# Kernel optimization log

Measured on AMD Instinct MI355X. Metric: run time of the kernel, lower is better.

The kernel has to match this reference:

```python
import jax, jax.numpy as jnp
import numpy as np

B = 16384          # batch_size / n_samples
SRC = 200          # source_num
C = 10             # category_size
I = SRC * C        # input_size = 2000
EPS = 1e-10


def setup_inputs() -> dict:
    key = jax.random.key(0)
    ks = jax.random.split(key, 8)
    # forward data
    x = jax.random.uniform(ks[0], (B, I), dtype=jnp.float32)
    mask = jax.random.uniform(ks[1], (B, I), dtype=jnp.float32)
    y_target = jax.random.uniform(ks[2], (B, C), dtype=jnp.float32)
    # learned parameters (xavier-uniform style init)
    def xavier(k, shape):
        fan_in, fan_out = shape[0], shape[1]
        limit = float(np.sqrt(2.0)) * float(np.sqrt(6.0 / (fan_in + fan_out)))
        return jax.random.uniform(k, shape, dtype=jnp.float32, minval=-limit, maxval=limit)
    W_reconstr = xavier(ks[3], (C, I))
    b_reconstr = xavier(ks[4], (1, I))
    W_yc = xavier(ks[5], (I, C))
    b_yc = xavier(ks[6], (1, C))
    return {"x": x, "mask": mask, "y_target": y_target,
            "W_reconstr": W_reconstr, "b_reconstr": b_reconstr,
            "W_yc": W_yc, "b_yc": b_yc}


def reference(x, mask, y_target, W_reconstr, b_reconstr, W_yc, b_yc):
    # ---- decoder (collapsed): constant_y[i] is a batch of identical one-hot
    # rows at category i, so y @ W_reconstr + b == W_reconstr[i] + b for all
    # batch elements. Stack over all i -> logits [C, I].
    logits = W_reconstr + b_reconstr                      # [C, I]
    e = jnp.exp(logits).reshape(C, SRC, C)                # per-source blocks
    # block-diagonal matmul == segmented sum over each source's C entries
    p = (e / e.sum(axis=-1, keepdims=True)).reshape(C, I)  # [C, I]
    logp = jnp.log(EPS + p)                               # [C, I]
    # -mean_j(mask * x * log p_i) per category i -> [B, C]
    reconstr_x = -(x * mask) @ logp.T / I

    # ---- encoder
    y_classifier = jax.nn.softmax(x @ W_yc + b_yc, axis=1)  # [B, C]

    # ---- losses
    loss_w_l1 = jnp.sum(jnp.abs(W_yc))
    loss_classifier_y_x = jnp.mean(jnp.sum(y_classifier * reconstr_x, axis=1))
    loss_y_kl = jnp.mean(jnp.sum(
        y_classifier * (jnp.log(EPS + y_classifier) - jnp.log(EPS + y_target)),
        axis=1))
    loss = (loss_classifier_y_x + 1e-4 * loss_y_kl
            + 0.005 / SRC / C / C * loss_w_l1)
    return (y_classifier, loss)
```

## Files before the change

kernel.cpp:

```cpp
#include <hip/hip_runtime.h>
#include <hip/hip_bf16.h>

#define B_SZ 16384
#define SRCN 200
#define CAT  10
#define IN   2000
#define QCOL 500
#define QPAD 512
#define TQB  10240
#define EPSF 1e-10f

typedef _Float16 half2v __attribute__((ext_vector_type(2)));

#if __has_builtin(__builtin_amdgcn_fdot2)
__device__ __forceinline__ float fdot2(half2v a, half2v b, float c) {
    return __builtin_amdgcn_fdot2(a, b, c, false);
}
#else
__device__ __forceinline__ float fdot2(half2v a, half2v b, float c) {
    return c + (float)a[0] * (float)b[0] + (float)a[1] * (float)b[1];
}
#endif

__device__ __forceinline__ half2v pkrtz(float a, float b) {
#if __has_builtin(__builtin_amdgcn_cvt_pkrtz)
    union { __fp16 __attribute__((ext_vector_type(2))) i; half2v o; } v;
    v.i = __builtin_amdgcn_cvt_pkrtz(a, b);
    return v.o;
#else
    half2v r; r[0] = (_Float16)a; r[1] = (_Float16)b; return r;
#endif
}

__device__ __forceinline__ half2v as_h2(unsigned u) {
    union { unsigned u; half2v h; } v; v.u = u; return v.h;
}

__device__ __forceinline__ short f2h(float f) {
    union { _Float16 h; short s; } v; v.h = (_Float16)f; return v.s;
}

__global__ void prep_kernel(const float* __restrict__ W_rec,
                            const float* __restrict__ b_rec,
                            const float* __restrict__ W_yc,
                            short* __restrict__ lp4,
                            short* __restrict__ wy4,
                            double* __restrict__ acc) {
    if (blockIdx.x == gridDim.x - 1) {
        float p = 0.f;
        for (int i = threadIdx.x; i < IN * CAT; i += blockDim.x) p += fabsf(W_yc[i]);
        __shared__ float red[4];
        for (int o = 32; o; o >>= 1) p += __shfl_down(p, o, 64);
        if ((threadIdx.x & 63) == 0) red[threadIdx.x >> 6] = p;
        __syncthreads();
        if (threadIdx.x == 0) {
            acc[0] = 0.0; acc[1] = 0.0;
            acc[2] = (double)(red[0] + red[1] + red[2] + red[3]);
        }
        return;
    }
    int idx = blockIdx.x * blockDim.x + threadIdx.x;
    int q   = idx / (CAT * QPAD);
    int rem = idx % (CAT * QPAD);
    int n   = rem >> 9;
    int kk  = rem & 511;
    short wv = 0, lv = 0;
    if (kk < QCOL) {
        int k = q * QCOL + kk;
        wv = f2h(W_yc[k * CAT + n]);
        int base = (k / CAT) * CAT;
        float lg[CAT];
        float m = -1e30f;
        #pragma unroll
        for (int i = 0; i < CAT; i++) {
            lg[i] = W_rec[n * IN + base + i] + b_rec[base + i];
            m = fmaxf(m, lg[i]);
        }
        float s = 0.f;
        #pragma unroll
        for (int i = 0; i < CAT; i++) s += expf(lg[i] - m);
        float myl = W_rec[n * IN + k] + b_rec[k];
        float pp = expf(myl - m) / s;
        lv = f2h(logf(EPSF + pp));
    }
    lp4[idx] = lv;
    wy4[idx] = wv;
}

__global__ __launch_bounds__(256, 4) void main_kernel(
        const float* __restrict__ x, const float* __restrict__ mask,
        const short* __restrict__ lp4, const short* __restrict__ wy4,
        float* __restrict__ part) {
    __shared__ __attribute__((aligned(16))) char lds[2 * TQB];

    const int q = blockIdx.x & 3;
    {
        const uint4* s1 = (const uint4*)(lp4 + q * (CAT * QPAD));
        const uint4* s2 = (const uint4*)(wy4 + q * (CAT * QPAD));
        uint4* d1 = (uint4*)lds;
        uint4* d2 = (uint4*)(lds + TQB);
        #pragma unroll
        for (int i = 0; i < 3; ++i) {
            int j = i * 256 + threadIdx.x;
            if (j < 640) { d1[j] = s1[j]; d2[j] = s2[j]; }
        }
    }
    __syncthreads();

    const int l  = threadIdx.x & 63;
    const int w  = threadIdx.x >> 6;
    const int g  = l >> 4;
    const int li = l & 15;
    const int row = (blockIdx.x >> 2) * 16 + w * 4 + g;

    const int col0 = q * QCOL + li * 4;
    const float* xr = x + (size_t)row * IN + col0;
    const float* mr = mask + (size_t)row * IN + col0;

    float4 xv[8], mv[8];
    #pragma unroll
    for (int cc = 0; cc < 7; ++cc) {
        xv[cc] = *(const float4*)(xr + cc * 64);
        mv[cc] = *(const float4*)(mr + cc * 64);
    }
    {
        const int base = col0 + 7 * 64;
        const int adj = (base > IN - 4) ? (base - (IN - 4)) : 0;
        xv[7] = *(const float4*)(xr + 7 * 64 - adj);
        mv[7] = *(const float4*)(mr + 7 * 64 - adj);
    }

    float pR[CAT], pW[CAT];
    #pragma unroll
    for (int c = 0; c < CAT; ++c) { pR[c] = 0.f; pW[c] = 0.f; }

    #pragma unroll
    for (int cc = 0; cc < 8; ++cc) {
        const half2v ax0 = pkrtz(xv[cc].x, xv[cc].y);
        const half2v ax1 = pkrtz(xv[cc].z, xv[cc].w);
        const half2v am0 = pkrtz(xv[cc].x * mv[cc].x, xv[cc].y * mv[cc].y);
        const half2v am1 = pkrtz(xv[cc].z * mv[cc].z, xv[cc].w * mv[cc].w);
        const int tb = cc * 128 + li * 8;
        #pragma unroll
        for (int c = 0; c < CAT; ++c) {
            const uint2 lpv = *(const uint2*)(lds + c * 1024 + tb);
            const uint2 wyv = *(const uint2*)(lds + TQB + c * 1024 + tb);
            pR[c] = fdot2(am0, as_h2(lpv.x), pR[c]);
            pR[c] = fdot2(am1, as_h2(lpv.y), pR[c]);
            pW[c] = fdot2(ax0, as_h2(wyv.x), pW[c]);
            pW[c] = fdot2(ax1, as_h2(wyv.y), pW[c]);
        }
    }

    #pragma unroll
    for (int c = 0; c < CAT; ++c) {
        #pragma unroll
        for (int o = 1; o < 16; o <<= 1) {
            pR[c] += __shfl_xor(pR[c], o, 64);
            pW[c] += __shfl_xor(pW[c], o, 64);
        }
    }
    if (li == 0) {
        float* pp = part + ((size_t)row * 4 + q) * 20;
        #pragma unroll
        for (int c = 0; c < CAT; ++c) { pp[c] = pR[c]; pp[10 + c] = pW[c]; }
    }
}

__global__ void combine_kernel(const float* __restrict__ part,
                               const float* __restrict__ y_target,
                               const float* __restrict__ b_yc,
                               float* __restrict__ out,
                               double* __restrict__ acc) {
    const int row = blockIdx.x * 256 + threadIdx.x;
    const float* pp = part + (size_t)row * 80;
    float pR[CAT], pW[CAT];
    #pragma unroll
    for (int c = 0; c < CAT; ++c) {
        pR[c] = pp[c] + pp[20 + c] + pp[40 + c] + pp[60 + c];
        pW[c] = pp[10 + c] + pp[30 + c] + pp[50 + c] + pp[70 + c] + b_yc[c];
    }
    float mx = -1e30f;
    #pragma unroll
    for (int c = 0; c < CAT; ++c) mx = fmaxf(mx, pW[c]);
    float y[CAT], s = 0.f;
    #pragma unroll
    for (int c = 0; c < CAT; ++c) { y[c] = __expf(pW[c] - mx); s += y[c]; }
    const float is = 1.f / s;
    float cls = 0.f, kl = 0.f;
    float* op = out + (size_t)row * CAT;
    #pragma unroll
    for (int c = 0; c < CAT; ++c) {
        y[c] *= is;
        op[c] = y[c];
        cls += y[c] * (-pR[c] * (1.f / IN));
        const float yt = y_target[(size_t)row * CAT + c];
        kl += y[c] * (__logf(EPSF + y[c]) - __logf(EPSF + yt));
    }
    #pragma unroll
    for (int o = 32; o; o >>= 1) {
        cls += __shfl_down(cls, o, 64);
        kl  += __shfl_down(kl, o, 64);
    }
    __shared__ float rc[4], rk[4];
    if ((threadIdx.x & 63) == 0) {
        rc[threadIdx.x >> 6] = cls; rk[threadIdx.x >> 6] = kl;
    }
    __syncthreads();
    if (threadIdx.x == 0) {
        atomicAdd(&acc[0], (double)(rc[0] + rc[1] + rc[2] + rc[3]));
        atomicAdd(&acc[1], (double)(rk[0] + rk[1] + rk[2] + rk[3]));
    }
}

__global__ void final_kernel(const double* __restrict__ acc,
                             float* __restrict__ out) {
    if (threadIdx.x == 0) {
        double loss = acc[0] / (double)B_SZ
                    + 1e-4 * (acc[1] / (double)B_SZ)
                    + (0.005 / (double)SRCN / (double)CAT / (double)CAT) * acc[2];
        out[(size_t)B_SZ * CAT] = (float)loss;
    }
}

extern "C" void kernel_launch(void* const* d_in, const int* in_sizes, int n_in,
                              void* d_out, int out_size, void* d_ws, size_t ws_size,
                              hipStream_t stream) {
    const float* x        = (const float*)d_in[0];
    const float* mask     = (const float*)d_in[1];
    const float* y_target = (const float*)d_in[2];
    const float* W_rec    = (const float*)d_in[3];
    const float* b_rec    = (const float*)d_in[4];
    const float* W_yc     = (const float*)d_in[5];
    const float* b_yc     = (const float*)d_in[6];
    float* out  = (float*)d_out;
    double* acc = (double*)d_ws;
    short* lp4  = (short*)((char*)d_ws + 256);
    short* wy4  = lp4 + 4 * CAT * QPAD;
    float* part = (float*)((char*)d_ws + 256 + 2 * 40960);

    prep_kernel<<<81, 256, 0, stream>>>(W_rec, b_rec, W_yc, lp4, wy4, acc);
    main_kernel<<<4096, 256, 0, stream>>>(x, mask, lp4, wy4, part);
    combine_kernel<<<64, 256, 0, stream>>>(part, y_target, b_yc, out, acc);
    final_kernel<<<1, 64, 0, stream>>>(acc, out);
}
```

Measured before the change: 72.99 us.

## Persistent-style main kernel with double-buffered row-tile prefetch

The main kernel drops from 4096 to 1024 blocks, and each block now handles four row tiles in a loop. The x and mask loads are split into two halves that are double-buffered, so the next tile's global loads are issued while the current half computes. Scheduling barriers pin the order. This spreads the LDS table staging over more work and hides memory latency, at the cost of higher register pressure and fewer blocks in flight.

```diff
diff --git a/kernel.cpp b/kernel.cpp
--- a/kernel.cpp
+++ b/kernel.cpp
@@ -8,6 +8,7 @@
 #define QCOL 500
 #define QPAD 512
 #define TQB  10240
+#define NBLK 1024
 #define EPSF 1e-10f
 
 typedef _Float16 half2v __attribute__((ext_vector_type(2)));
@@ -111,59 +112,88 @@
     const int w  = threadIdx.x >> 6;
     const int g  = l >> 4;
     const int li = l & 15;
-    const int row = (blockIdx.x >> 2) * 16 + w * 4 + g;
-
+    const int rt0 = blockIdx.x >> 2;
     const int col0 = q * QCOL + li * 4;
-    const float* xr = x + (size_t)row * IN + col0;
-    const float* mr = mask + (size_t)row * IN + col0;
-
-    float4 xv[8], mv[8];
-    #pragma unroll
-    for (int cc = 0; cc < 7; ++cc) {
-        xv[cc] = *(const float4*)(xr + cc * 64);
-        mv[cc] = *(const float4*)(mr + cc * 64);
-    }
-    {
-        const int base = col0 + 7 * 64;
-        const int adj = (base > IN - 4) ? (base - (IN - 4)) : 0;
-        xv[7] = *(const float4*)(xr + 7 * 64 - adj);
-        mv[7] = *(const float4*)(mr + 7 * 64 - adj);
-    }
-
+
+    auto rowOf = [&](int t) { return (rt0 + t * 256) * 16 + w * 4 + g; };
+
+    auto issue = [&](float4* xv, float4* mv, int t, int hb) {
+        const float* xr = x + (size_t)rowOf(t) * IN + col0;
+        const float* mr = mask + (size_t)rowOf(t) * IN + col0;
+        #pragma unroll
+        for (int j = 0; j < 4; ++j) {
+            const int cc = hb + j;
+            int off = cc * 64;
+            if (cc == 7) {
+                const int base = col0 + 448;
+                off -= (base > IN - 4) ? (base - (IN - 4)) : 0;
+            }
+            xv[j] = *(const float4*)(xr + off);
+            mv[j] = *(const float4*)(mr + off);
+        }
+    };
+
+    auto compute = [&](const float4* xv, const float4* mv, int hb,
+                       float* pR, float* pW) {
+        #pragma unroll
+        for (int j = 0; j < 4; ++j) {
+            const int cc = hb + j;
+            const half2v ax0 = pkrtz(xv[j].x, xv[j].y);
+            const half2v ax1 = pkrtz(xv[j].z, xv[j].w);
+            const half2v am0 = pkrtz(xv[j].x * mv[j].x, xv[j].y * mv[j].y);
+            const half2v am1 = pkrtz(xv[j].z * mv[j].z, xv[j].w * mv[j].w);
+            const int tb = cc * 128 + li * 8;
+            #pragma unroll
+            for (int c = 0; c < CAT; ++c) {
+                const uint2 lpv = *(const uint2*)(lds + c * 1024 + tb);
+                const uint2 wyv = *(const uint2*)(lds + TQB + c * 1024 + tb);
+                pR[c] = fdot2(am0, as_h2(lpv.x), pR[c]);
+                pR[c] = fdot2(am1, as_h2(lpv.y), pR[c]);
+                pW[c] = fdot2(ax0, as_h2(wyv.x), pW[c]);
+                pW[c] = fdot2(ax1, as_h2(wyv.y), pW[c]);
+            }
+        }
+    };
+
+    auto reduceStore = [&](float* pR, float* pW, int t) {
+        #pragma unroll
+        for (int c = 0; c < CAT; ++c) {
+            #pragma unroll
+            for (int o = 1; o < 16; o <<= 1) {
+                pR[c] += __shfl_xor(pR[c], o, 64);
+                pW[c] += __shfl_xor(pW[c], o, 64);
+            }
+        }
+        if (li == 0) {
+            float* pp = part + ((size_t)rowOf(t) * 4 + q) * 20;
+            #pragma unroll
+            for (int c = 0; c < CAT; ++c) { pp[c] = pR[c]; pp[10 + c] = pW[c]; }
+        }
+    };
+
+    float4 xA[4], mA[4], xB[4], mB[4];
     float pR[CAT], pW[CAT];
-    #pragma unroll
-    for (int c = 0; c < CAT; ++c) { pR[c] = 0.f; pW[c] = 0.f; }
-
-    #pragma unroll
-    for (int cc = 0; cc < 8; ++cc) {
-        const half2v ax0 = pkrtz(xv[cc].x, xv[cc].y);
-        const half2v ax1 = pkrtz(xv[cc].z, xv[cc].w);
-        const half2v am0 = pkrtz(xv[cc].x * mv[cc].x, xv[cc].y * mv[cc].y);
-        const half2v am1 = pkrtz(xv[cc].z * mv[cc].z, xv[cc].w * mv[cc].w);
-        const int tb = cc * 128 + li * 8;
-        #pragma unroll
-        for (int c = 0; c < CAT; ++c) {
-            const uint2 lpv = *(const uint2*)(lds + c * 1024 + tb);
-            const uint2 wyv = *(const uint2*)(lds + TQB + c * 1024 + tb);
-            pR[c] = fdot2(am0, as_h2(lpv.x), pR[c]);
-            pR[c] = fdot2(am1, as_h2(lpv.y), pR[c]);
-            pW[c] = fdot2(ax0, as_h2(wyv.x), pW[c]);
-            pW[c] = fdot2(ax1, as_h2(wyv.y), pW[c]);
-        }
-    }
-
-    #pragma unroll
-    for (int c = 0; c < CAT; ++c) {
-        #pragma unroll
-        for (int o = 1; o < 16; o <<= 1) {
-            pR[c] += __shfl_xor(pR[c], o, 64);
-            pW[c] += __shfl_xor(pW[c], o, 64);
-        }
-    }
-    if (li == 0) {
-        float* pp = part + ((size_t)row * 4 + q) * 20;
-        #pragma unroll
-        for (int c = 0; c < CAT; ++c) { pp[c] = pR[c]; pp[10 + c] = pW[c]; }
+
+    issue(xA, mA, 0, 0);
+    issue(xB, mB, 0, 4);
+    __builtin_amdgcn_sched_barrier(0);
+
+    #pragma unroll
+    for (int t = 0; t < 4; ++t) {
+        #pragma unroll
+        for (int c = 0; c < CAT; ++c) { pR[c] = 0.f; pW[c] = 0.f; }
+
+        compute(xA, mA, 0, pR, pW);
+        if (t < 3) {
+            issue(xA, mA, t + 1, 0);
+            __builtin_amdgcn_sched_barrier(0);
+        }
+        compute(xB, mB, 4, pR, pW);
+        if (t < 3) {
+            issue(xB, mB, t + 1, 4);
+            __builtin_amdgcn_sched_barrier(0);
+        }
+        reduceStore(pR, pW, t);
     }
 }
 
@@ -240,7 +270,7 @@
     float* part = (float*)((char*)d_ws + 256 + 2 * 40960);
 
     prep_kernel<<<81, 256, 0, stream>>>(W_rec, b_rec, W_yc, lp4, wy4, acc);
-    main_kernel<<<4096, 256, 0, stream>>>(x, mask, lp4, wy4, part);
+    main_kernel<<<NBLK, 256, 0, stream>>>(x, mask, lp4, wy4, part);
     combine_kernel<<<64, 256, 0, stream>>>(part, y_target, b_yc, out, acc);
     final_kernel<<<1, 64, 0, stream>>>(acc, out);
 }
```

Result: slower. 124.5 us (+70.6%).

## Make main kernel persistent over four row tiles with inline-asm software-pipelined loads

Applied to the files above, without the earlier changes.

The main kernel now launches a quarter as many blocks, and each block processes four row tiles spaced 4096 rows apart. Global loads are issued with inline asm and explicit s_waitcnt so the next tile's x/mask loads overlap compute on the current half-tile. The LDS table load is amortised over four tiles and memory latency is meant to be hidden by double buffering. The cost is higher register pressure from the extra buffered float4s and fewer blocks for the scheduler to balance across CUs.

```diff
diff --git a/kernel.cpp b/kernel.cpp
--- a/kernel.cpp
+++ b/kernel.cpp
@@ -9,7 +9,9 @@
 #define QPAD 512
 #define TQB  10240
 #define EPSF 1e-10f
-
+#define TILESTRIDE 8192000
+
+typedef float f32x4 __attribute__((ext_vector_type(4)));
 typedef _Float16 half2v __attribute__((ext_vector_type(2)));
 
 #if __has_builtin(__builtin_amdgcn_fdot2)
@@ -111,35 +113,50 @@
     const int w  = threadIdx.x >> 6;
     const int g  = l >> 4;
     const int li = l & 15;
-    const int row = (blockIdx.x >> 2) * 16 + w * 4 + g;
+    const int row0 = (blockIdx.x >> 2) * 16 + w * 4 + g;
 
     const int col0 = q * QCOL + li * 4;
-    const float* xr = x + (size_t)row * IN + col0;
-    const float* mr = mask + (size_t)row * IN + col0;
-
-    float4 xv[8], mv[8];
-    #pragma unroll
-    for (int cc = 0; cc < 7; ++cc) {
-        xv[cc] = *(const float4*)(xr + cc * 64);
-        mv[cc] = *(const float4*)(mr + cc * 64);
-    }
-    {
-        const int base = col0 + 7 * 64;
-        const int adj = (base > IN - 4) ? (base - (IN - 4)) : 0;
-        xv[7] = *(const float4*)(xr + 7 * 64 - adj);
-        mv[7] = *(const float4*)(mr + 7 * 64 - adj);
-    }
+    const float* xr = x + (size_t)row0 * IN + col0;
+    const float* mr = mask + (size_t)row0 * IN + col0;
+    const int b7  = col0 + 448;
+    const int adj = (b7 > IN - 4) ? (b7 - (IN - 4)) : 0;
+
+    f32x4 XA0, XA1, XA2, XA3, MA0, MA1, MA2, MA3;
+    f32x4 XB0, XB1, XB2, XB3, MB0, MB1, MB2, MB3;
+
+    auto issueA = [&](int i) {
+        const float* xp = xr + (size_t)i * TILESTRIDE;
+        const float* mp = mr + (size_t)i * TILESTRIDE;
+        asm volatile("global_load_dwordx4 %0, %1, off"            : "=&v"(XA0) : "v"(xp) : "memory");
+        asm volatile("global_load_dwordx4 %0, %1, off"            : "=&v"(MA0) : "v"(mp) : "memory");
+        asm volatile("global_load_dwordx4 %0, %1, off offset:256" : "=&v"(XA1) : "v"(xp) : "memory");
+        asm volatile("global_load_dwordx4 %0, %1, off offset:256" : "=&v"(MA1) : "v"(mp) : "memory");
+        asm volatile("global_load_dwordx4 %0, %1, off offset:512" : "=&v"(XA2) : "v"(xp) : "memory");
+        asm volatile("global_load_dwordx4 %0, %1, off offset:512" : "=&v"(MA2) : "v"(mp) : "memory");
+        asm volatile("global_load_dwordx4 %0, %1, off offset:768" : "=&v"(XA3) : "v"(xp) : "memory");
+        asm volatile("global_load_dwordx4 %0, %1, off offset:768" : "=&v"(MA3) : "v"(mp) : "memory");
+    };
+    auto issueB = [&](int i) {
+        const float* xp = xr + (size_t)i * TILESTRIDE;
+        const float* mp = mr + (size_t)i * TILESTRIDE;
+        const float* x7 = xp + 448 - adj;
+        const float* m7 = mp + 448 - adj;
+        asm volatile("global_load_dwordx4 %0, %1, off offset:1024" : "=&v"(XB0) : "v"(xp) : "memory");
+        asm volatile("global_load_dwordx4 %0, %1, off offset:1024" : "=&v"(MB0) : "v"(mp) : "memory");
+        asm volatile("global_load_dwordx4 %0, %1, off offset:1280" : "=&v"(XB1) : "v"(xp) : "memory");
+        asm volatile("global_load_dwordx4 %0, %1, off offset:1280" : "=&v"(MB1) : "v"(mp) : "memory");
+        asm volatile("global_load_dwordx4 %0, %1, off offset:1536" : "=&v"(XB2) : "v"(xp) : "memory");
+        asm volatile("global_load_dwordx4 %0, %1, off offset:1536" : "=&v"(MB2) : "v"(mp) : "memory");
+        asm volatile("global_load_dwordx4 %0, %1, off"             : "=&v"(XB3) : "v"(x7) : "memory");
+        asm volatile("global_load_dwordx4 %0, %1, off"             : "=&v"(MB3) : "v"(m7) : "memory");
+    };
 
     float pR[CAT], pW[CAT];
-    #pragma unroll
-    for (int c = 0; c < CAT; ++c) { pR[c] = 0.f; pW[c] = 0.f; }
-
-    #pragma unroll
-    for (int cc = 0; cc < 8; ++cc) {
-        const half2v ax0 = pkrtz(xv[cc].x, xv[cc].y);
-        const half2v ax1 = pkrtz(xv[cc].z, xv[cc].w);
-        const half2v am0 = pkrtz(xv[cc].x * mv[cc].x, xv[cc].y * mv[cc].y);
-        const half2v am1 = pkrtz(xv[cc].z * mv[cc].z, xv[cc].w * mv[cc].w);
+    auto dochunk = [&](f32x4 xv, f32x4 mv, int cc) {
+        const half2v ax0 = pkrtz(xv[0], xv[1]);
+        const half2v ax1 = pkrtz(xv[2], xv[3]);
+        const half2v am0 = pkrtz(xv[0] * mv[0], xv[1] * mv[1]);
+        const half2v am1 = pkrtz(xv[2] * mv[2], xv[3] * mv[3]);
         const int tb = cc * 128 + li * 8;
         #pragma unroll
         for (int c = 0; c < CAT; ++c) {
@@ -150,20 +167,50 @@
             pW[c] = fdot2(ax0, as_h2(wyv.x), pW[c]);
             pW[c] = fdot2(ax1, as_h2(wyv.y), pW[c]);
         }
-    }
-
-    #pragma unroll
-    for (int c = 0; c < CAT; ++c) {
-        #pragma unroll
-        for (int o = 1; o < 16; o <<= 1) {
-            pR[c] += __shfl_xor(pR[c], o, 64);
-            pW[c] += __shfl_xor(pW[c], o, 64);
-        }
-    }
-    if (li == 0) {
-        float* pp = part + ((size_t)row * 4 + q) * 20;
-        #pragma unroll
-        for (int c = 0; c < CAT; ++c) { pp[c] = pR[c]; pp[10 + c] = pW[c]; }
+    };
+
+    issueA(0);
+    issueB(0);
+
+    #pragma unroll
+    for (int i = 0; i < 4; ++i) {
+        #pragma unroll
+        for (int c = 0; c < CAT; ++c) { pR[c] = 0.f; pW[c] = 0.f; }
+
+        asm volatile("s_waitcnt vmcnt(8)"
+                     : "+v"(XA0), "+v"(XA1), "+v"(XA2), "+v"(XA3),
+                       "+v"(MA0), "+v"(MA1), "+v"(MA2), "+v"(MA3));
+        dochunk(XA0, MA0, 0); dochunk(XA1, MA1, 1);
+        dochunk(XA2, MA2, 2); dochunk(XA3, MA3, 3);
+        if (i < 3) issueA(i + 1);
+
+        if (i < 3) {
+            asm volatile("s_waitcnt vmcnt(8)"
+                         : "+v"(XB0), "+v"(XB1), "+v"(XB2), "+v"(XB3),
+                           "+v"(MB0), "+v"(MB1), "+v"(MB2), "+v"(MB3));
+        } else {
+            asm volatile("s_waitcnt vmcnt(0)"
+                         : "+v"(XB0), "+v"(XB1), "+v"(XB2), "+v"(XB3),
+                           "+v"(MB0), "+v"(MB1), "+v"(MB2), "+v"(MB3));
+        }
+        dochunk(XB0, MB0, 4); dochunk(XB1, MB1, 5);
+        dochunk(XB2, MB2, 6); dochunk(XB3, MB3, 7);
+        if (i < 3) issueB(i + 1);
+
+        #pragma unroll
+        for (int c = 0; c < CAT; ++c) {
+            #pragma unroll
+            for (int o = 1; o < 16; o <<= 1) {
+                pR[c] += __shfl_xor(pR[c], o, 64);
+                pW[c] += __shfl_xor(pW[c], o, 64);
+            }
+        }
+        if (li == 0) {
+            const int rowi = row0 + i * 4096;
+            float* pp = part + ((size_t)rowi * 4 + q) * 20;
+            #pragma unroll
+            for (int c = 0; c < CAT; ++c) { pp[c] = pR[c]; pp[10 + c] = pW[c]; }
+        }
     }
 }
 
@@ -240,7 +287,7 @@
     float* part = (float*)((char*)d_ws + 256 + 2 * 40960);
 
     prep_kernel<<<81, 256, 0, stream>>>(W_rec, b_rec, W_yc, lp4, wy4, acc);
-    main_kernel<<<4096, 256, 0, stream>>>(x, mask, lp4, wy4, part);
+    main_kernel<<<1024, 256, 0, stream>>>(x, mask, lp4, wy4, part);
     combine_kernel<<<64, 256, 0, stream>>>(part, y_target, b_yc, out, acc);
     final_kernel<<<1, 64, 0, stream>>>(acc, out);
 }
```

Measured after the change: 79.20 us. 8.5% more time.
